# Optimization experiments

Hardware: AMD Instinct MI355X
Metric: run time of the kernel (lower is better)

## Reference

```python
import jax, jax.numpy as jnp
import numpy as np
import math

K = 1.0          # Lorentz manifold curvature param: points satisfy <x,x>_L = -K
NUM_HEADS = 16
EPS = 1e-6
B, L, D = 2, 2048, 1024


def lorentz_inner(x, y):
    # <x,y>_L = -x0*y0 + sum_{i>0} xi*yi  (over last dim)
    return jnp.sum(x * y, axis=-1) - 2.0 * x[..., 0] * y[..., 0]


def project_to_lorentz(z):
    # treat z[...,1:] as space components, recompute time so <x,x>_L = -K
    space = z[..., 1:]
    time = jnp.sqrt(K + jnp.sum(space * space, axis=-1, keepdims=True))
    return jnp.concatenate([time, space], axis=-1)


def hlinear(x, W, b, num_heads):
    # Lorentz linear layer (Chen et al. 2022): Euclidean affine map on the
    # ambient coordinates followed by curvature-aware time re-normalization.
    z = x @ W.T + b  # (B, L, D)
    if num_heads > 0:
        Bz, Lz, Dz = z.shape
        z = z.reshape(Bz, Lz, num_heads, Dz // num_heads)  # (B, L, H, dh)
    return project_to_lorentz(z)


def setup_inputs() -> dict:
    key = jax.random.key(0)
    ks = jax.random.split(key, 8)
    def mk_point(k):
        # random manifold points: random space part, valid time coordinate
        z = jax.random.normal(k, (B, L, D), dtype=jnp.float32) * 0.5
        return project_to_lorentz(z)
    scale = 1.0 / math.sqrt(D)
    def mk_w(k):
        return jax.random.normal(k, (D, D), dtype=jnp.float32) * scale
    return {
        "query": mk_point(ks[0]),
        "key": mk_point(ks[1]),
        "value": mk_point(ks[2]),
        "W_Q": mk_w(ks[3]), "b_Q": jnp.zeros((D,), jnp.float32),
        "W_K": mk_w(ks[4]), "b_K": jnp.zeros((D,), jnp.float32),
        "W_V": mk_w(ks[5]), "b_V": jnp.zeros((D,), jnp.float32),
        "W_O": mk_w(ks[6]), "b_O": jnp.zeros((D,), jnp.float32),
    }


def reference(query, key, value, W_Q, b_Q, W_K, b_K, W_V, b_V, W_O, b_O):
    H = NUM_HEADS
    q = hlinear(query, W_Q, b_Q, H)  # (B, L, H, dh) on per-head Lorentz manifold
    k = hlinear(key, W_K, b_K, H)
    v = hlinear(value, W_V, b_V, H)
    dh = q.shape[-1]
    # Lorentzian inner products <q_i, k_j>_L per head: (B, H, Lq, Lk)
    ip = (jnp.einsum('bqhd,bkhd->bhqk', q, k)
          - 2.0 * jnp.einsum('bqh,bkh->bhqk', q[..., 0], k[..., 0]))
    # negative squared Lorentz distance: -d_L^2 = 2K + 2<q,k>_L, scaled by sqrt(dh)
    scores = (2.0 * K + 2.0 * ip) * (1.0 / math.sqrt(dh))
    attn = jax.nn.softmax(scores, axis=-1)
    # Lorentzian centroid aggregation (Law et al.): normalize weighted sum back
    # onto the hyperboloid.
    mu = jnp.einsum('bhqk,bkhd->bqhd', attn, v)  # (B, L, H, dh)
    norm = jnp.sqrt(jnp.maximum(jnp.abs(lorentz_inner(mu, mu)), EPS))
    out_heads = math.sqrt(K) * mu / norm[..., None]
    cat = out_heads.reshape(out_heads.shape[0], out_heads.shape[1], -1)  # (B, L, D)
    return hlinear(cat, W_O, b_O, 0)  # (B, L, D) on the manifold
```

## Files before the change

kernel.cpp:

```cpp
#include <hip/hip_runtime.h>
#include <math.h>

namespace {
constexpr int Ln = 2048;
constexpr int Dn = 1024;
constexpr int Mn = 4096;
constexpr float QSCALE = 0.25f * 1.44269504088896340736f;
}

typedef unsigned short u16;
typedef unsigned int u32;
typedef __attribute__((ext_vector_type(4))) float f32x4;
typedef __attribute__((ext_vector_type(8))) __bf16 bf16x8;
typedef __attribute__((ext_vector_type(4))) unsigned short u16x4;
typedef __attribute__((ext_vector_type(8))) unsigned short u16x8;
typedef __attribute__((ext_vector_type(4))) unsigned int u32x4;


__device__ __forceinline__ u16 f2bf(float f) {
    union { float f; unsigned u; } cv; cv.f = f;
    unsigned u = cv.u + 0x7fffu + ((cv.u >> 16) & 1u);
    return (u16)(u >> 16);
}
__device__ __forceinline__ float bf2f(u16 h) {
    union { unsigned u; float f; } cv; cv.u = ((unsigned)h) << 16;
    return cv.f;
}

__device__ __forceinline__ u32 pkbf(float a, float b) {
    union { __bf16 h[2]; u32 u; } cv;
    cv.h[0] = (__bf16)a; cv.h[1] = (__bf16)b;
    return cv.u;
}

#if __has_builtin(__builtin_amdgcn_exp2f)
__device__ __forceinline__ float exp2_fast(float x) {
    return __builtin_amdgcn_exp2f(x);
}
#else
__device__ __forceinline__ float exp2_fast(float x) {
    float r;
    asm("v_exp_f32 %0, %1" : "=v"(r) : "v"(x));
    return r;
}
#endif

template <int CTRL>
__device__ __forceinline__ float dppf(float x) {
    return __int_as_float(__builtin_amdgcn_update_dpp(
        0, __float_as_int(x), CTRL, 0xf, 0xf, true));
}
__device__ __forceinline__ float red16_add(float x) {
    x += dppf<0xB1>(x);
    x += dppf<0x4E>(x);
    x += dppf<0x141>(x);
    x += dppf<0x140>(x);
    return x;
}

__device__ __forceinline__ void gload16(const void* g, void* l) {
    __builtin_amdgcn_global_load_lds(
        (const __attribute__((address_space(1))) unsigned int*)g,
        (__attribute__((address_space(3))) unsigned int*)l, 16, 0, 0);
}

__global__ __launch_bounds__(256)
void cvt_in3(const float* __restrict__ i0, const float* __restrict__ i1,
             const float* __restrict__ i2,
             u16* __restrict__ o0, u16* __restrict__ o1, u16* __restrict__ o2)
{
    const int z = blockIdx.y;
    const float* in = z == 0 ? i0 : (z == 1 ? i1 : i2);
    u16* out       = z == 0 ? o0 : (z == 1 ? o1 : o2);
    int i = blockIdx.x * 256 + threadIdx.x;
    f32x4 v = ((const f32x4*)in)[i];
    u16x4 o;
#pragma unroll
    for (int j = 0; j < 4; ++j) o[j] = f2bf(v[j]);
    int l = i >> 8;
    int e = (i & 255) * 4;
    int idx = l * 1024 + (e & ~63) + (((((e >> 3) & 7) ^ (l & 7))) << 3) + (e & 7);
    *(u16x4*)&out[idx] = o;
}

__global__ __launch_bounds__(256)
void cvt_w(const float* __restrict__ w0, const float* __restrict__ w1,
           const float* __restrict__ w2, const float* __restrict__ w3,
           u16* __restrict__ q0, u16* __restrict__ q1,
           u16* __restrict__ q2, u16* __restrict__ q3)
{
    const int z = blockIdx.y;
    int i = blockIdx.x * 256 + threadIdx.x;
    if (z < 3) {
        const float* in = z == 0 ? w0 : (z == 1 ? w1 : w2);
        u16* out       = z == 0 ? q0 : (z == 1 ? q1 : q2);
        f32x4 v = ((const f32x4*)in)[i];
        u16x4 o;
#pragma unroll
        for (int j = 0; j < 4; ++j) o[j] = f2bf(v[j]);
        int l = i >> 8;
        int e = (i & 255) * 4;
        int idx = l * 1024 + (e & ~63) + (((((e >> 3) & 7) ^ (l & 7))) << 3) + (e & 7);
        *(u16x4*)&out[idx] = o;
    } else {
        int o  = i >> 8;
        int s0 = (i & 255) * 4;
        int h = s0 >> 6, sl = s0 & 63, a = sl >> 2;
        const float* src = w3 + (size_t)o * 1024 + h * 64;
        u16x4 ov = { f2bf(src[a]), f2bf(src[16 + a]),
                     f2bf(src[32 + a]), f2bf(src[48 + a]) };
        int idx = o * 1024 + h * 64 + (((sl >> 3) ^ (o & 7)) << 3) + (sl & 7);
        *(u16x4*)&q3[idx] = ov;
    }
}

__global__ __launch_bounds__(256)
void gemm_qkv(const u16* __restrict__ xq, const u16* __restrict__ xk,
              const u16* __restrict__ xv, const u16* __restrict__ wq,
              const u16* __restrict__ wk, const u16* __restrict__ wv,
              const float* __restrict__ bq, const float* __restrict__ bk,
              const float* __restrict__ bv,
              u16* __restrict__ oq, u16* __restrict__ ok, u16* __restrict__ ov)
{
    const int t = threadIdx.x;
    const int lane = t & 63, w = t >> 6;
    const int g = lane >> 4, c = lane & 15;
    const int wr = w >> 1, wc = w & 1;
    const int id = blockIdx.x;
    const int bm = (id & 31) * 128;
    const int bn = ((id >> 5) & 7) * 128;
    const int z  = id >> 8;

    const u16* A = z == 0 ? xq : (z == 1 ? xk : xv);
    const u16* W = z == 0 ? wq : (z == 1 ? wk : wv);
    const float* bias = z == 0 ? bq : (z == 1 ? bk : bv);
    u16* Ct = z == 0 ? oq : (z == 1 ? ok : ov);
    const float scale = z == 0 ? QSCALE : 1.f;
    const float tsign = z == 0 ? -1.f : 1.f;

    const int s7 = c & 7;
    const int ko0 = ((0 + g) ^ s7) << 3;
    const int ko1 = ((4 + g) ^ s7) << 3;
    const u16* Ab[4];
    const u16* Bb[4];
#pragma unroll
    for (int mi = 0; mi < 4; ++mi)
        Ab[mi] = A + (size_t)(bm + wr * 64 + mi * 16 + c) * Dn;
#pragma unroll
    for (int ni = 0; ni < 4; ++ni)
        Bb[ni] = W + (size_t)(bn + wc * 64 + ni * 16 + c) * Dn;

    f32x4 acc[4][4];
    const f32x4 z4 = {0.f, 0.f, 0.f, 0.f};
#pragma unroll
    for (int i = 0; i < 4; ++i)
#pragma unroll
        for (int j = 0; j < 4; ++j) acc[i][j] = z4;

    bf16x8 a0[4], b0[4], a1[4], b1[4];
#pragma unroll
    for (int mi = 0; mi < 4; ++mi) a0[mi] = *(const bf16x8*)(Ab[mi] + ko0);
#pragma unroll
    for (int ni = 0; ni < 4; ++ni) b0[ni] = *(const bf16x8*)(Bb[ni] + ko0);

    for (int ki = 0; ki < 16; ++ki) {
        const int kb = ki * 64;
#pragma unroll
        for (int mi = 0; mi < 4; ++mi) a1[mi] = *(const bf16x8*)(Ab[mi] + kb + ko1);
#pragma unroll
        for (int ni = 0; ni < 4; ++ni) b1[ni] = *(const bf16x8*)(Bb[ni] + kb + ko1);
        __builtin_amdgcn_s_setprio(1);
#pragma unroll
        for (int mi = 0; mi < 4; ++mi)
#pragma unroll
            for (int ni = 0; ni < 4; ++ni)
                acc[mi][ni] = __builtin_amdgcn_mfma_f32_16x16x32_bf16(
                    a0[mi], b0[ni], acc[mi][ni], 0, 0, 0);
        __builtin_amdgcn_s_setprio(0);
        if (ki + 1 < 16) {
#pragma unroll
            for (int mi = 0; mi < 4; ++mi)
                a0[mi] = *(const bf16x8*)(Ab[mi] + kb + 64 + ko0);
#pragma unroll
            for (int ni = 0; ni < 4; ++ni)
                b0[ni] = *(const bf16x8*)(Bb[ni] + kb + 64 + ko0);
        }
        __builtin_amdgcn_s_setprio(1);
#pragma unroll
        for (int mi = 0; mi < 4; ++mi)
#pragma unroll
            for (int ni = 0; ni < 4; ++ni)
                acc[mi][ni] = __builtin_amdgcn_mfma_f32_16x16x32_bf16(
                    a1[mi], b1[ni], acc[mi][ni], 0, 0, 0);
        __builtin_amdgcn_s_setprio(0);
    }

    const int hcb = bn + wc * 64;
    const int h = hcb >> 6;
#pragma unroll
    for (int mi = 0; mi < 4; ++mi)
#pragma unroll
        for (int j = 0; j < 4; ++j) {
            int ll = bm + wr * 64 + mi * 16 + g * 4 + j;
            float zv[4];
#pragma unroll
            for (int ni = 0; ni < 4; ++ni)
                zv[ni] = acc[mi][ni][j] + bias[hcb + ni * 16 + c];
            float loc = zv[0]*zv[0] + zv[1]*zv[1] + zv[2]*zv[2] + zv[3]*zv[3];
            if (c == 0) loc -= zv[0] * zv[0];
            loc = red16_add(loc);
            float tval = sqrtf(1.f + loc);
            float v0 = (c == 0) ? tsign * tval : zv[0];
            int bb = ll >> 11, l2 = ll & 2047;
            u16* dst = Ct + (((size_t)bb * 16 + h) * Ln + l2) * 64;
            u16x4 pkv = { f2bf(v0 * scale), f2bf(zv[1] * scale),
                          f2bf(zv[2] * scale), f2bf(zv[3] * scale) };
            *(u16x4*)&dst[(4 * c) ^ ((ll & 7) << 3)] = pkv;
        }
}

__global__ __launch_bounds__(256)
void transpose_v(const u16* __restrict__ vin, u16* __restrict__ vout)
{
    __shared__ u16 raw[64 * 64];
    const int t = threadIdx.x;
    const int bh = blockIdx.x, lc = blockIdx.y;
    const u16* src = vin + ((size_t)bh * Ln + lc * 64) * 64;
#pragma unroll
    for (int p = 0; p < 2; ++p) {
        int ci = p * 256 + t;
        *(u16x8*)&raw[ci * 8] = *(const u16x8*)(src + ci * 8);
    }
    __syncthreads();
    const int d = t >> 2, cp0 = (t & 3) * 16;
    const int s = ((d & 15) << 2) | (d >> 4);
    u16 buf[16];
#pragma unroll
    for (int i = 0; i < 16; ++i) {
        int cp = cp0 + i;
        int n = ((cp >> 5) << 5) | (((cp >> 2) & 1) << 4) | (((cp >> 3) & 3) << 2) | (cp & 3);
        buf[i] = raw[n * 64 + ((((s >> 3) ^ (n & 7)) << 3) | (s & 7))];
    }
    u16* dst = vout + ((size_t)bh * 64 + d) * Ln + lc * 64;
    int b0 = cp0 >> 3;
    *(u16x8*)&dst[((b0 ^ (d & 7)) << 3)]       = *(const u16x8*)&buf[0];
    *(u16x8*)&dst[(((b0 + 1) ^ (d & 7)) << 3)] = *(const u16x8*)&buf[8];
}

__global__ __launch_bounds__(256, 4)
void attn_mfma(const u16* __restrict__ qt, const u16* __restrict__ kt,
               const u16* __restrict__ vT, u16* __restrict__ part)
{
    __shared__ u16 smem[4 * 4096];

    const int t = threadIdx.x;
    const int lane = t & 63, w = t >> 6;
    const int g = lane >> 4, c = lane & 15;
    const int id  = blockIdx.x;
    const int qb  = (id >> 3) & 15;
    const int gidx = (id & 7) | ((id >> 7) << 3);
    const int bh  = gidx & 31;
    const int kvh = gidx >> 5;
    const int q0  = qb * 128;
    const u16* Q = qt + (size_t)bh * Ln * 64;
    const u16* K = kt + (size_t)bh * Ln * 64 + (size_t)kvh * (1024 * 64);
    const u16* V = vT + (size_t)bh * 64 * (size_t)Ln + kvh * 1024;

    bf16x8 qa[2][2];
#pragma unroll
    for (int mi = 0; mi < 2; ++mi)
#pragma unroll
        for (int kk = 0; kk < 2; ++kk) {
            int row = q0 + w * 32 + mi * 16 + c;
            qa[mi][kk] = *(const bf16x8*)(Q + (size_t)row * 64 +
                                          (((kk * 4 + g) ^ (c & 7)) << 3));
        }

    f32x4 o[2][4];
    const f32x4 z4 = {0.f, 0.f, 0.f, 0.f};
#pragma unroll
    for (int mi = 0; mi < 2; ++mi)
#pragma unroll
        for (int di = 0; di < 4; ++di) o[mi][di] = z4;

    const int fb0 = c * 128 + (((0 + g) ^ (c & 7)) << 4);
    const int fb1 = c * 128 + (((4 + g) ^ (c & 7)) << 4);

    char* sb = (char*)smem;
    const int cr = t >> 3, cb = t & 7;
    const u16* kp = K + (size_t)cr * 64 + cb * 8;
    const u16* vp = V + (size_t)cr * Ln + cb * 8;

    gload16(kp,            sb + t * 16);
    gload16(kp + 2048,     sb + 4096 + t * 16);
    gload16(vp,            sb + 16384 + t * 16);
    gload16(vp + 32 * Ln,  sb + 16384 + 4096 + t * 16);

    constexpr int NC = 1024 / 64;
    for (int ch = 0; ch < NC; ++ch) {
        __syncthreads();
        if (ch + 1 < NC) {
            const u16* kn = kp + (ch + 1) * 4096;
            const u16* vn = vp + (ch + 1) * 64;
            char* db = sb + (((ch + 1) & 1) << 13);
            gload16(kn,           db + t * 16);
            gload16(kn + 2048,    db + 4096 + t * 16);
            gload16(vn,           db + 16384 + t * 16);
            gload16(vn + 32 * Ln, db + 16384 + 4096 + t * 16);
        }
        const char* kbb = sb + ((ch & 1) << 13);
        const char* vbb = kbb + 16384;

        f32x4 sf[2][4];
#pragma unroll
        for (int mi = 0; mi < 2; ++mi)
#pragma unroll
            for (int ni = 0; ni < 4; ++ni) sf[mi][ni] = z4;
        __builtin_amdgcn_s_setprio(1);
#pragma unroll
        for (int kk = 0; kk < 2; ++kk) {
            const int fb = kk ? fb1 : fb0;
            bf16x8 kb[4];
#pragma unroll
            for (int ni = 0; ni < 4; ++ni)
                kb[ni] = *(const bf16x8*)(kbb + fb + ni * 2048);
#pragma unroll
            for (int mi = 0; mi < 2; ++mi)
#pragma unroll
                for (int ni = 0; ni < 4; ++ni)
                    sf[mi][ni] = __builtin_amdgcn_mfma_f32_16x16x32_bf16(
                        kb[ni], qa[mi][kk], sf[mi][ni], 0, 0, 0);
        }
        __builtin_amdgcn_s_setprio(0);

        bf16x8 paf[2][2];
#pragma unroll
        for (int mi = 0; mi < 2; ++mi) {
            float ex[4][4];
#pragma unroll
            for (int ni = 0; ni < 4; ++ni)
#pragma unroll
                for (int j = 0; j < 4; ++j)
                    ex[ni][j] = exp2_fast(sf[mi][ni][j]);
            u32x4 p0 = { pkbf(ex[0][0], ex[0][1]), pkbf(ex[0][2], ex[0][3]),
                         pkbf(ex[1][0], ex[1][1]), pkbf(ex[1][2], ex[1][3]) };
            u32x4 p1 = { pkbf(ex[2][0], ex[2][1]), pkbf(ex[2][2], ex[2][3]),
                         pkbf(ex[3][0], ex[3][1]), pkbf(ex[3][2], ex[3][3]) };
            paf[mi][0] = __builtin_bit_cast(bf16x8, p0);
            paf[mi][1] = __builtin_bit_cast(bf16x8, p1);
        }

        __builtin_amdgcn_s_setprio(1);
#pragma unroll
        for (int kk = 0; kk < 2; ++kk) {
            const int fb = kk ? fb1 : fb0;
#pragma unroll
            for (int di = 0; di < 4; ++di) {
                bf16x8 vb = *(const bf16x8*)(vbb + fb + di * 2048);
#pragma unroll
                for (int mi = 0; mi < 2; ++mi)
                    o[mi][di] = __builtin_amdgcn_mfma_f32_16x16x32_bf16(
                        paf[mi][kk], vb, o[mi][di], 0, 0, 0);
            }
        }
        __builtin_amdgcn_s_setprio(0);
    }

    u16* P = part + (size_t)(kvh * 32 + bh) * (4 * 2048 * 16);
#pragma unroll
    for (int mi = 0; mi < 2; ++mi)
#pragma unroll
        for (int j = 0; j < 4; ++j) {
            int row = q0 + w * 32 + mi * 16 + g * 4 + j;
#pragma unroll
            for (int di = 0; di < 4; ++di)
                P[(di * 2048 + row) * 16 + c] = f2bf(o[mi][di][j]);
        }
}

__global__ __launch_bounds__(256)
void attn_combine(const u16* __restrict__ part, u16* __restrict__ cat)
{
    const int grp = blockIdx.x * 16 + (threadIdx.x >> 4);
    const int c = threadIdx.x & 15;
    const int bh = grp >> 11, q = grp & 2047;
    const u16* P0 = part + (size_t)bh * (4 * 2048 * 16);
    const u16* P1 = part + (size_t)(32 + bh) * (4 * 2048 * 16);
    float mu[4];
#pragma unroll
    for (int di = 0; di < 4; ++di) {
        int idx = (di * 2048 + q) * 16 + c;
        mu[di] = bf2f(P0[idx]) + bf2f(P1[idx]);
    }
    float loc = mu[0]*mu[0] + mu[1]*mu[1] + mu[2]*mu[2] + mu[3]*mu[3];
    if (c == 0) loc -= 2.f * mu[0] * mu[0];
    loc = red16_add(loc);
    float rn = rsqrtf(fmaxf(fabsf(loc), 1e-6f));
    const int b = bh >> 4, h = bh & 15;
    u16* dst = cat + ((size_t)b * Ln + q) * Dn + h * 64;
    u16x4 pkv = { f2bf(mu[0] * rn), f2bf(mu[1] * rn),
                  f2bf(mu[2] * rn), f2bf(mu[3] * rn) };
    *(u16x4*)&dst[(4 * c) ^ ((q & 7) << 3)] = pkv;
}

__global__ __launch_bounds__(256)
void gemm_o(const u16* __restrict__ A, const u16* __restrict__ B,
            const float* __restrict__ bias, float* __restrict__ C)
{
    __shared__ u16 As[2][64 * 64];
    __shared__ u16 Bs[2][128 * 64];
    const int t = threadIdx.x;
    const int lane = t & 63, w = t >> 6;
    const int g = lane >> 4, c = lane & 15;
    const int wr = w >> 1, wc = w & 1;
    const int id = blockIdx.x;
    const int bm = ((id & 7) * 8 + ((id >> 3) & 7)) * 64;
    const int bn = (id >> 6) * 128;

    f32x4 acc[2][4];
    const f32x4 z4 = {0.f, 0.f, 0.f, 0.f};
#pragma unroll
    for (int i = 0; i < 2; ++i)
#pragma unroll
        for (int j = 0; j < 4; ++j) acc[i][j] = z4;

    const int sr = t >> 3, sb2 = (t & 7) * 8;
    const u16* Ap = A + (size_t)(bm + sr) * Dn + sb2;
    const u16* Bp = B + (size_t)(bn + sr) * Dn + sb2;

    auto stage = [&](int buf, int k0) {
        gload16(Ap + k0,            &As[buf][t * 8]);
        gload16(Ap + 32 * Dn + k0,  &As[buf][(256 + t) * 8]);
        gload16(Bp + k0,            &Bs[buf][t * 8]);
        gload16(Bp + 32 * Dn + k0,  &Bs[buf][(256 + t) * 8]);
        gload16(Bp + 64 * Dn + k0,  &Bs[buf][(512 + t) * 8]);
        gload16(Bp + 96 * Dn + k0,  &Bs[buf][(768 + t) * 8]);
    };

    stage(0, 0);
    for (int ki = 0; ki < 16; ++ki) {
        __syncthreads();
        if (ki + 1 < 16) stage((ki + 1) & 1, (ki + 1) * 64);
        const u16* as = As[ki & 1];
        const u16* bs = Bs[ki & 1];
#pragma unroll
        for (int kk = 0; kk < 2; ++kk) {
            const int so = ((kk * 4 + g) ^ (c & 7)) << 3;
            bf16x8 a[2], b[4];
#pragma unroll
            for (int mi = 0; mi < 2; ++mi)
                a[mi] = *(const bf16x8*)&as[(wr * 32 + mi * 16 + c) * 64 + so];
#pragma unroll
            for (int ni = 0; ni < 4; ++ni)
                b[ni] = *(const bf16x8*)&bs[(wc * 64 + ni * 16 + c) * 64 + so];
            __builtin_amdgcn_s_setprio(1);
#pragma unroll
            for (int mi = 0; mi < 2; ++mi)
#pragma unroll
                for (int ni = 0; ni < 4; ++ni)
                    acc[mi][ni] = __builtin_amdgcn_mfma_f32_16x16x32_bf16(
                        a[mi], b[ni], acc[mi][ni], 0, 0, 0);
            __builtin_amdgcn_s_setprio(0);
        }
    }

#pragma unroll
    for (int mi = 0; mi < 2; ++mi)
#pragma unroll
        for (int j = 0; j < 4; ++j) {
            size_t row = bm + wr * 32 + mi * 16 + g * 4 + j;
#pragma unroll
            for (int ni = 0; ni < 4; ++ni) {
                int col = bn + wc * 64 + ni * 16 + c;
                C[row * Dn + col] = acc[mi][ni][j] + bias[col];
            }
        }
}

__global__ __launch_bounds__(256)
void lorentz_row_full(float* __restrict__ z)
{
    __shared__ float red[4];
    const int t = threadIdx.x;
    const size_t base = (size_t)blockIdx.x * Dn;
    float4 v = *(const float4*)&z[base + t * 4];
    if (t == 0) v.x = 0.f;
    float ssq = v.x * v.x + v.y * v.y + v.z * v.z + v.w * v.w;
#pragma unroll
    for (int off = 32; off; off >>= 1) ssq += __shfl_xor(ssq, off);
    if ((t & 63) == 0) red[t >> 6] = ssq;
    __syncthreads();
    if (t == 0) z[base] = sqrtf(1.0f + red[0] + red[1] + red[2] + red[3]);
}

extern "C" void kernel_launch(void* const* d_in, const int* in_sizes, int n_in,
                              void* d_out, int out_size, void* d_ws, size_t ws_size,
                              hipStream_t stream)
{
    const float* query = (const float*)d_in[0];
    const float* key_  = (const float*)d_in[1];
    const float* value = (const float*)d_in[2];
    const float* W_Q   = (const float*)d_in[3];
    const float* b_Q   = (const float*)d_in[4];
    const float* W_K   = (const float*)d_in[5];
    const float* b_K   = (const float*)d_in[6];
    const float* W_V   = (const float*)d_in[7];
    const float* b_V   = (const float*)d_in[8];
    const float* W_O   = (const float*)d_in[9];
    const float* b_O   = (const float*)d_in[10];

    const size_t MD = (size_t)Mn * Dn;
    const size_t DD = (size_t)Dn * Dn;
    u16* xq   = (u16*)d_ws;
    u16* xk   = xq + MD;
    u16* xv   = xk + MD;
    u16* wo   = xv + MD;
    u16* q_t  = wo + DD;
    u16* k_t  = q_t + MD;
    u16* wq   = k_t + MD;
    u16* wk   = wq + DD;
    u16* wv   = wk + DD;
    u16* v_ln = wv + DD;
    u16* part = wq;
    u16* v_T  = xv;
    u16* cat  = xk;

    dim3 ci(Mn * Dn / 1024, 3);
    cvt_in3<<<ci, 256, 0, stream>>>(query, key_, value, xq, xk, xv);
    dim3 cw(Dn * Dn / 1024, 4);
    cvt_w<<<cw, 256, 0, stream>>>(W_Q, W_K, W_V, W_O, wq, wk, wv, wo);

    gemm_qkv<<<768, 256, 0, stream>>>(xq, xk, xv, wq, wk, wv,
                                      b_Q, b_K, b_V, q_t, k_t, v_ln);

    dim3 tg(32, Ln / 64);
    transpose_v<<<tg, 256, 0, stream>>>(v_ln, v_T);

    attn_mfma<<<1024, 256, 0, stream>>>(q_t, k_t, v_T, part);

    attn_combine<<<4096, 256, 0, stream>>>(part, cat);

    gemm_o<<<512, 256, 0, stream>>>(cat, wo, b_O, (float*)d_out);
    lorentz_row_full<<<Mn, 256, 0, stream>>>((float*)d_out);
}
```

Baseline: 129.2 us.

## Load K/V fragments directly from global in attention, double rows per warp

The attention kernel drops its double-buffered LDS staging of K and V tiles and the per-chunk barriers. Each lane now loads its MFMA fragments straight from global memory, relying on the pre-swizzled layouts. Each warp covers 64 query rows instead of 32, which halves the grid to 512 blocks and doubles K/V reuse per load. The QKV GEMM k-loop is also fully unrolled. In exchange, register pressure rises (more accumulators, no occupancy hint), occupancy and block count fall, and global loads are no longer prefetched ahead of use.

```diff
diff --git a/kernel.cpp b/kernel.cpp
--- a/kernel.cpp
+++ b/kernel.cpp
@@ -163,6 +163,7 @@
 #pragma unroll
     for (int ni = 0; ni < 4; ++ni) b0[ni] = *(const bf16x8*)(Bb[ni] + ko0);
 
+#pragma unroll
     for (int ki = 0; ki < 16; ++ki) {
         const int kb = ki * 64;
 #pragma unroll
@@ -247,95 +248,78 @@
     *(u16x8*)&dst[(((b0 + 1) ^ (d & 7)) << 3)] = *(const u16x8*)&buf[8];
 }
 
-__global__ __launch_bounds__(256, 4)
+__global__ __launch_bounds__(256)
 void attn_mfma(const u16* __restrict__ qt, const u16* __restrict__ kt,
                const u16* __restrict__ vT, u16* __restrict__ part)
 {
-    __shared__ u16 smem[4 * 4096];
-
     const int t = threadIdx.x;
     const int lane = t & 63, w = t >> 6;
     const int g = lane >> 4, c = lane & 15;
     const int id  = blockIdx.x;
-    const int qb  = (id >> 3) & 15;
-    const int gidx = (id & 7) | ((id >> 7) << 3);
+    const int qb  = (id >> 3) & 7;
+    const int gidx = (id & 7) | ((id >> 6) << 3);
     const int bh  = gidx & 31;
     const int kvh = gidx >> 5;
-    const int q0  = qb * 128;
+    const int q0  = qb * 256;
     const u16* Q = qt + (size_t)bh * Ln * 64;
     const u16* K = kt + (size_t)bh * Ln * 64 + (size_t)kvh * (1024 * 64);
     const u16* V = vT + (size_t)bh * 64 * (size_t)Ln + kvh * 1024;
 
-    bf16x8 qa[2][2];
-#pragma unroll
-    for (int mi = 0; mi < 2; ++mi)
+    const int s7 = c & 7;
+    const int ko0 = ((0 + g) ^ s7) << 3;
+    const int ko1 = ((4 + g) ^ s7) << 3;
+
+    bf16x8 qa[4][2];
+#pragma unroll
+    for (int mi = 0; mi < 4; ++mi) {
+        int row = q0 + w * 64 + mi * 16 + c;
+        qa[mi][0] = *(const bf16x8*)(Q + (size_t)row * 64 + ko0);
+        qa[mi][1] = *(const bf16x8*)(Q + (size_t)row * 64 + ko1);
+    }
+
+    const u16* KB[4];
+    const u16* VB[4];
+#pragma unroll
+    for (int ni = 0; ni < 4; ++ni) KB[ni] = K + (size_t)(ni * 16 + c) * 64;
+#pragma unroll
+    for (int di = 0; di < 4; ++di) VB[di] = V + (size_t)(di * 16 + c) * Ln;
+
+    f32x4 o[4][4];
+    const f32x4 z4 = {0.f, 0.f, 0.f, 0.f};
+#pragma unroll
+    for (int mi = 0; mi < 4; ++mi)
+#pragma unroll
+        for (int di = 0; di < 4; ++di) o[mi][di] = z4;
+
+    for (int ch = 0; ch < 16; ++ch) {
+        const int kof = ch * 4096;
+        const int vof = ch * 64;
+
+        f32x4 sf[4][4];
+#pragma unroll
+        for (int mi = 0; mi < 4; ++mi)
+#pragma unroll
+            for (int ni = 0; ni < 4; ++ni) sf[mi][ni] = z4;
 #pragma unroll
         for (int kk = 0; kk < 2; ++kk) {
-            int row = q0 + w * 32 + mi * 16 + c;
-            qa[mi][kk] = *(const bf16x8*)(Q + (size_t)row * 64 +
-                                          (((kk * 4 + g) ^ (c & 7)) << 3));
-        }
-
-    f32x4 o[2][4];
-    const f32x4 z4 = {0.f, 0.f, 0.f, 0.f};
-#pragma unroll
-    for (int mi = 0; mi < 2; ++mi)
-#pragma unroll
-        for (int di = 0; di < 4; ++di) o[mi][di] = z4;
-
-    const int fb0 = c * 128 + (((0 + g) ^ (c & 7)) << 4);
-    const int fb1 = c * 128 + (((4 + g) ^ (c & 7)) << 4);
-
-    char* sb = (char*)smem;
-    const int cr = t >> 3, cb = t & 7;
-    const u16* kp = K + (size_t)cr * 64 + cb * 8;
-    const u16* vp = V + (size_t)cr * Ln + cb * 8;
-
-    gload16(kp,            sb + t * 16);
-    gload16(kp + 2048,     sb + 4096 + t * 16);
-    gload16(vp,            sb + 16384 + t * 16);
-    gload16(vp + 32 * Ln,  sb + 16384 + 4096 + t * 16);
-
-    constexpr int NC = 1024 / 64;
-    for (int ch = 0; ch < NC; ++ch) {
-        __syncthreads();
-        if (ch + 1 < NC) {
-            const u16* kn = kp + (ch + 1) * 4096;
-            const u16* vn = vp + (ch + 1) * 64;
-            char* db = sb + (((ch + 1) & 1) << 13);
-            gload16(kn,           db + t * 16);
-            gload16(kn + 2048,    db + 4096 + t * 16);
-            gload16(vn,           db + 16384 + t * 16);
-            gload16(vn + 32 * Ln, db + 16384 + 4096 + t * 16);
-        }
-        const char* kbb = sb + ((ch & 1) << 13);
-        const char* vbb = kbb + 16384;
-
-        f32x4 sf[2][4];
-#pragma unroll
-        for (int mi = 0; mi < 2; ++mi)
-#pragma unroll
-            for (int ni = 0; ni < 4; ++ni) sf[mi][ni] = z4;
-        __builtin_amdgcn_s_setprio(1);
-#pragma unroll
-        for (int kk = 0; kk < 2; ++kk) {
-            const int fb = kk ? fb1 : fb0;
+            const int ko = kk ? ko1 : ko0;
             bf16x8 kb[4];
 #pragma unroll
             for (int ni = 0; ni < 4; ++ni)
-                kb[ni] = *(const bf16x8*)(kbb + fb + ni * 2048);
-#pragma unroll
-            for (int mi = 0; mi < 2; ++mi)
+                kb[ni] = *(const bf16x8*)(KB[ni] + kof + ko);
+            __builtin_amdgcn_s_setprio(1);
+#pragma unroll
+            for (int mi = 0; mi < 4; ++mi)
 #pragma unroll
                 for (int ni = 0; ni < 4; ++ni)
                     sf[mi][ni] = __builtin_amdgcn_mfma_f32_16x16x32_bf16(
                         kb[ni], qa[mi][kk], sf[mi][ni], 0, 0, 0);
-        }
-        __builtin_amdgcn_s_setprio(0);
-
-        bf16x8 paf[2][2];
-#pragma unroll
-        for (int mi = 0; mi < 2; ++mi) {
+            __builtin_amdgcn_s_setprio(0);
+        }
+
+        bf16x8 paf[4][2];
+#pragma unroll
+        for (int mi = 0; mi < 4; ++mi) {
             float ex[4][4];
 #pragma unroll
             for (int ni = 0; ni < 4; ++ni)
@@ -350,28 +334,30 @@
             paf[mi][1] = __builtin_bit_cast(bf16x8, p1);
         }
 
-        __builtin_amdgcn_s_setprio(1);
 #pragma unroll
         for (int kk = 0; kk < 2; ++kk) {
-            const int fb = kk ? fb1 : fb0;
-#pragma unroll
-            for (int di = 0; di < 4; ++di) {
-                bf16x8 vb = *(const bf16x8*)(vbb + fb + di * 2048);
-#pragma unroll
-                for (int mi = 0; mi < 2; ++mi)
+            const int ko = kk ? ko1 : ko0;
+            bf16x8 vb[4];
+#pragma unroll
+            for (int di = 0; di < 4; ++di)
+                vb[di] = *(const bf16x8*)(VB[di] + vof + ko);
+            __builtin_amdgcn_s_setprio(1);
+#pragma unroll
+            for (int di = 0; di < 4; ++di)
+#pragma unroll
+                for (int mi = 0; mi < 4; ++mi)
                     o[mi][di] = __builtin_amdgcn_mfma_f32_16x16x32_bf16(
-                        paf[mi][kk], vb, o[mi][di], 0, 0, 0);
-            }
-        }
-        __builtin_amdgcn_s_setprio(0);
+                        paf[mi][kk], vb[di], o[mi][di], 0, 0, 0);
+            __builtin_amdgcn_s_setprio(0);
+        }
     }
 
     u16* P = part + (size_t)(kvh * 32 + bh) * (4 * 2048 * 16);
 #pragma unroll
-    for (int mi = 0; mi < 2; ++mi)
+    for (int mi = 0; mi < 4; ++mi)
 #pragma unroll
         for (int j = 0; j < 4; ++j) {
-            int row = q0 + w * 32 + mi * 16 + g * 4 + j;
+            int row = q0 + w * 64 + mi * 16 + g * 4 + j;
 #pragma unroll
             for (int di = 0; di < 4; ++di)
                 P[(di * 2048 + row) * 16 + c] = f2bf(o[mi][di][j]);
@@ -536,7 +522,7 @@
     dim3 tg(32, Ln / 64);
     transpose_v<<<tg, 256, 0, stream>>>(v_ln, v_T);
 
-    attn_mfma<<<1024, 256, 0, stream>>>(q_t, k_t, v_T, part);
+    attn_mfma<<<512, 256, 0, stream>>>(q_t, k_t, v_T, part);
 
     attn_combine<<<4096, 256, 0, stream>>>(part, cat);
 
```

Measured after the change: 137.3 us. 1.06x slower.
